# Optimization experiments

Hardware: AMD Instinct MI355X
Metric: run time of the kernel (lower is better)

Reference implementation:

```python
import jax, jax.numpy as jnp
import numpy as np

MOE_TOP_K = 2
MOE_GATE_NORM_STD = 1.0  # moe_gate_norm_std


def setup_inputs() -> dict:
    key = jax.random.key(0)
    k1, k2, k3, k4 = jax.random.split(key, 4)
    T, D, E = 16384, 2048, 8
    return {
        "x": jax.random.normal(k1, (T, D), dtype=jnp.float32),
        "wg_weight": jax.random.normal(k2, (E, D), dtype=jnp.float32) * 0.02,
        "gate_map_weight": jax.random.normal(k3, (E, E), dtype=jnp.float32) * 0.1,
        "gate_residual": jax.random.normal(k4, (T, E), dtype=jnp.float32),
    }


def reference(x, wg_weight, gate_map_weight, gate_residual):
    # Router GEMM in fp32 (module force-casts wg and input to float32)
    logits = jnp.einsum("td,ed->te", x.astype(jnp.float32), wg_weight)  # [T, E]
    # gate_residual path: gate_map Linear(E, E, bias=False)
    logits = logits + jnp.einsum("te,fe->tf", gate_residual, gate_map_weight)

    num_experts = wg_weight.shape[0]
    # gating(): moe_use_mixtral_gating=False, moe_use_logits_norm=True
    # torch.std is unbiased (ddof=1)
    logits_std = jnp.std(logits, axis=1, keepdims=True, ddof=1)
    probs = jax.nn.softmax(logits / (logits_std / MOE_GATE_NORM_STD), axis=1)
    gates, indices = jax.lax.top_k(probs, MOE_TOP_K)  # [T, K]
    # zero out routing to the last expert, then renormalize
    gates = jnp.where(indices == num_experts - 1, jnp.zeros_like(gates), gates)
    gates = gates / jnp.sum(gates, axis=1, keepdims=True)
    # Dense equivalent of the per-expert nonzero-gather dict: (indices, gates)
    # fully determines expert_info[e] = (tokens where indices==e, matching gates).
    return gates, indices, logits
```

## Files before the change

kernel.cpp:

```cpp
#include <hip/hip_runtime.h>
#include <hip/hip_bf16.h>
#include <stdint.h>


#define DCONST 2048
#define TOK_PER_BATCH 8
#define BATCHES 4

typedef float f32x4 __attribute__((ext_vector_type(4)));

__device__ __forceinline__ unsigned long long shfl_xor_u64(unsigned long long v, int m) {
    int lo = __shfl_xor((int)(uint32_t)v, m, 64);
    int hi = __shfl_xor((int)(uint32_t)(v >> 32), m, 64);
    return ((unsigned long long)(uint32_t)hi << 32) | (unsigned long long)(uint32_t)lo;
}

__global__ __launch_bounds__(256, 2)
void router_gemm(const float* __restrict__ x,
                 const float* __restrict__ wg,
                 float* __restrict__ ws,
                 int T)
{
    const int wave  = threadIdx.x >> 6;
    const int lane  = threadIdx.x & 63;
    const int W     = blockIdx.x * 4 + wave;
    const int g     = W & 7;
    const int tbase = (W >> 3) * 32;

    const float* wgp = wg + g * 256 + (lane << 2);
    f32x4 w8[8];
    #pragma unroll
    for (int e = 0; e < 8; ++e)
        w8[e] = *(const f32x4*)(wgp + (size_t)e * DCONST);

    const float* xp = x + (size_t)tbase * DCONST + g * 256 + (lane << 2);

    f32x4 xa[4], xb[4];

    #define LOADH(buf, trow)                                                  \
        { _Pragma("unroll")                                                   \
          for (int i = 0; i < 4; ++i)                                         \
              buf[i] = __builtin_nontemporal_load(                            \
                  (const f32x4*)(xp + (size_t)((trow) + i) * DCONST)); }

    #define FMAH(buf, tloc0)                                                  \
        { _Pragma("unroll")                                                   \
          for (int i = 0; i < 4; ++i) {                                       \
              _Pragma("unroll")                                               \
              for (int e = 0; e < 8; ++e) {                                   \
                  float a = acc[((tloc0) + i) * 8 + e];                       \
                  a += buf[i].x * w8[e].x;                                    \
                  a += buf[i].y * w8[e].y;                                    \
                  a += buf[i].z * w8[e].z;                                    \
                  a += buf[i].w * w8[e].w;                                    \
                  acc[((tloc0) + i) * 8 + e] = a;                             \
              }                                                               \
          } }

    LOADH(xa, 0);
    LOADH(xb, 4);

    #pragma unroll 1
    for (int b = 0; b < BATCHES; ++b) {
        float acc[64];
        #pragma unroll
        for (int v = 0; v < 64; ++v) acc[v] = 0.f;

        FMAH(xa, 0);
        if (b < BATCHES - 1) LOADH(xa, (b + 1) * 8);
        FMAH(xb, 4);
        if (b < BATCHES - 1) LOADH(xb, (b + 1) * 8 + 4);

        #pragma unroll
        for (int m = 1; m < 64; m <<= 1) {
            const bool up = (lane & m) != 0;
            #pragma unroll
            for (int v = 0; v < 64; v += 2 * m) {
                const float keep = up ? acc[v + m] : acc[v];
                const float send = up ? acc[v] : acc[v + m];
                const float got  = __shfl_xor(send, m, 64);
                acc[v] = keep + got;
            }
        }

        const int tb = (tbase + b * TOK_PER_BATCH) >> 3;
        ws[(size_t)tb * 512 + g * 64 + lane] = acc[0];
    }
}

__global__ __launch_bounds__(256)
void router_epilogue(const float* __restrict__ ws,
                     const float* __restrict__ gm,
                     const float* __restrict__ gr,
                     float* __restrict__ out,
                     int T)
{
    const int wave = threadIdx.x >> 6;
    const int lane = threadIdx.x & 63;
    const int tb   = blockIdx.x * 4 + wave;
    const int t0   = tb * 8;

    float logit = 0.f;
    #pragma unroll
    for (int g = 0; g < 8; ++g)
        logit += ws[(size_t)tb * 512 + g * 64 + lane];

    const int tt = lane >> 3;
    const int f  = lane & 7;
    const int t  = t0 + tt;

    const float4 ga = *(const float4*)(gr + (size_t)t * 8);
    const float4 gb = *(const float4*)(gr + (size_t)t * 8 + 4);
    const float4 ma = *(const float4*)(gm + f * 8);
    const float4 mb = *(const float4*)(gm + f * 8 + 4);
    logit += ga.x * ma.x + ga.y * ma.y + ga.z * ma.z + ga.w * ma.w
           + gb.x * mb.x + gb.y * mb.y + gb.z * mb.z + gb.w * mb.w;

    out[(size_t)4 * T + (size_t)t0 * 8 + lane] = logit;

    float s = logit;
    s += __shfl_xor(s, 1, 64);
    s += __shfl_xor(s, 2, 64);
    s += __shfl_xor(s, 4, 64);
    const float mean = s * 0.125f;
    float d2 = (logit - mean) * (logit - mean);
    d2 += __shfl_xor(d2, 1, 64);
    d2 += __shfl_xor(d2, 2, 64);
    d2 += __shfl_xor(d2, 4, 64);
    const float stdv = sqrtf(d2 / 7.0f);

    uint32_t ob = __float_as_uint(logit);
    ob = (ob & 0x80000000u) ? ~ob : (ob | 0x80000000u);
    unsigned long long k1 = ((unsigned long long)ob << 8) | (unsigned long long)(7 - f);
    unsigned long long k2 = 0ull;
    #pragma unroll
    for (int m = 1; m <= 4; m <<= 1) {
        const unsigned long long o1 = shfl_xor_u64(k1, m);
        const unsigned long long o2 = shfl_xor_u64(k2, m);
        const unsigned long long hi = k1 > o1 ? k1 : o1;
        const unsigned long long lo = k1 > o1 ? o1 : k1;
        const unsigned long long so = k2 > o2 ? k2 : o2;
        k1 = hi;
        k2 = lo > so ? lo : so;
    }
    const int i1 = 7 - (int)(k1 & 0xFFull);
    const int i2 = 7 - (int)(k2 & 0xFFull);
    uint32_t b1 = (uint32_t)(k1 >> 8), b2 = (uint32_t)(k2 >> 8);
    b1 = (b1 & 0x80000000u) ? (b1 ^ 0x80000000u) : ~b1;
    b2 = (b2 & 0x80000000u) ? (b2 ^ 0x80000000u) : ~b2;
    const float l1 = __uint_as_float(b1);
    const float l2 = __uint_as_float(b2);

    float g0, g1;
    if (i1 == 7)      { g0 = 0.f; g1 = 1.f; }
    else if (i2 == 7) { g0 = 1.f; g1 = 0.f; }
    else {
        const float p = 1.0f / (1.0f + __expf(-(l1 - l2) / stdv));
        g0 = p; g1 = 1.0f - p;
    }

    if (f == 0) out[(size_t)2 * t]             = g0;
    if (f == 1) out[(size_t)2 * t + 1]         = g1;
    if (f == 2) out[(size_t)2 * T + 2 * t]     = (float)i1;
    if (f == 3) out[(size_t)2 * T + 2 * t + 1] = (float)i2;
}

extern "C" void kernel_launch(void* const* d_in, const int* in_sizes, int n_in,
                              void* d_out, int out_size, void* d_ws, size_t ws_size,
                              hipStream_t stream) {
    const float* x  = (const float*)d_in[0];
    const float* wg = (const float*)d_in[1];
    const float* gm = (const float*)d_in[2];
    const float* gr = (const float*)d_in[3];
    float* ws = (float*)d_ws;
    const int T = in_sizes[0] / DCONST;

    const int gemm_blocks = (8 * (T / 32)) / 4;
    router_gemm<<<gemm_blocks, 256, 0, stream>>>(x, wg, ws, T);

    const int epi_blocks = T / 32;
    router_epilogue<<<epi_blocks, 256, 0, stream>>>(ws, gm, gr, (float*)d_out, T);
}
```

Baseline: 189.9 us.

## Make router GEMM persistent with two work items per wave and double-buffered 8-row loads

The router GEMM grid is cut to a fixed 512 blocks, and each wave loops over two work items spaced 2048 waves apart. Within a work item, loads are now double-buffered across two 8-row buffers, so the next batch's loads are issued before the current batch's FMAs and shuffle reduction. The aim is more memory requests in flight per wave and less launch/tail overhead. In exchange it uses more registers (16 f32x4 buffers plus 64 accumulators), which may lower occupancy, and the hardcoded grid and stride assume T=16384.

```diff
diff --git a/kernel.cpp b/kernel.cpp
--- a/kernel.cpp
+++ b/kernel.cpp
@@ -4,8 +4,6 @@
 
 
 #define DCONST 2048
-#define TOK_PER_BATCH 8
-#define BATCHES 4
 
 typedef float f32x4 __attribute__((ext_vector_type(4)));
 
@@ -21,70 +19,70 @@
                  float* __restrict__ ws,
                  int T)
 {
-    const int wave  = threadIdx.x >> 6;
-    const int lane  = threadIdx.x & 63;
-    const int W     = blockIdx.x * 4 + wave;
-    const int g     = W & 7;
-    const int tbase = (W >> 3) * 32;
-
-    const float* wgp = wg + g * 256 + (lane << 2);
-    f32x4 w8[8];
-    #pragma unroll
-    for (int e = 0; e < 8; ++e)
-        w8[e] = *(const f32x4*)(wgp + (size_t)e * DCONST);
-
-    const float* xp = x + (size_t)tbase * DCONST + g * 256 + (lane << 2);
-
-    f32x4 xa[4], xb[4];
-
-    #define LOADH(buf, trow)                                                  \
-        { _Pragma("unroll")                                                   \
-          for (int i = 0; i < 4; ++i)                                         \
-              buf[i] = __builtin_nontemporal_load(                            \
-                  (const f32x4*)(xp + (size_t)((trow) + i) * DCONST)); }
-
-    #define FMAH(buf, tloc0)                                                  \
-        { _Pragma("unroll")                                                   \
-          for (int i = 0; i < 4; ++i) {                                       \
-              _Pragma("unroll")                                               \
-              for (int e = 0; e < 8; ++e) {                                   \
-                  float a = acc[((tloc0) + i) * 8 + e];                       \
-                  a += buf[i].x * w8[e].x;                                    \
-                  a += buf[i].y * w8[e].y;                                    \
-                  a += buf[i].z * w8[e].z;                                    \
-                  a += buf[i].w * w8[e].w;                                    \
-                  acc[((tloc0) + i) * 8 + e] = a;                             \
-              }                                                               \
-          } }
-
-    LOADH(xa, 0);
-    LOADH(xb, 4);
+    const int wave = threadIdx.x >> 6;
+    const int lane = threadIdx.x & 63;
+    const int W    = blockIdx.x * 4 + wave;
 
     #pragma unroll 1
-    for (int b = 0; b < BATCHES; ++b) {
-        float acc[64];
+    for (int s = 0; s < 2; ++s) {
+        const int id    = W + s * 2048;
+        const int g     = id & 7;
+        const int trow  = (id >> 3) * 32;
+        const int tb0   = trow >> 3;
+
+        const float* wgp = wg + g * 256 + (lane << 2);
+        f32x4 w8[8];
         #pragma unroll
-        for (int v = 0; v < 64; ++v) acc[v] = 0.f;
+        for (int e = 0; e < 8; ++e)
+            w8[e] = *(const f32x4*)(wgp + (size_t)e * DCONST);
 
-        FMAH(xa, 0);
-        if (b < BATCHES - 1) LOADH(xa, (b + 1) * 8);
-        FMAH(xb, 4);
-        if (b < BATCHES - 1) LOADH(xb, (b + 1) * 8 + 4);
+        const float* xp = x + (size_t)trow * DCONST + g * 256 + (lane << 2);
 
-        #pragma unroll
-        for (int m = 1; m < 64; m <<= 1) {
-            const bool up = (lane & m) != 0;
-            #pragma unroll
-            for (int v = 0; v < 64; v += 2 * m) {
-                const float keep = up ? acc[v + m] : acc[v];
-                const float send = up ? acc[v] : acc[v + m];
-                const float got  = __shfl_xor(send, m, 64);
-                acc[v] = keep + got;
-            }
+        f32x4 A[8], B[8];
+
+        #define LOADB(buf, b)                                                 \
+            { _Pragma("unroll")                                               \
+              for (int i = 0; i < 8; ++i)                                     \
+                  buf[i] = __builtin_nontemporal_load(                        \
+                      (const f32x4*)(xp + (size_t)((b) * 8 + i) * DCONST)); }
+
+        #define DOBATCH(buf, b)                                               \
+            { float acc[64];                                                  \
+              _Pragma("unroll")                                               \
+              for (int v = 0; v < 64; ++v) acc[v] = 0.f;                      \
+              _Pragma("unroll")                                               \
+              for (int i = 0; i < 8; ++i) {                                   \
+                  _Pragma("unroll")                                           \
+                  for (int e = 0; e < 8; ++e) {                               \
+                      float a = acc[i * 8 + e];                               \
+                      a += buf[i].x * w8[e].x;                                \
+                      a += buf[i].y * w8[e].y;                                \
+                      a += buf[i].z * w8[e].z;                                \
+                      a += buf[i].w * w8[e].w;                                \
+                      acc[i * 8 + e] = a;                                     \
+                  }                                                           \
+              }                                                               \
+              _Pragma("unroll")                                               \
+              for (int m = 1; m < 64; m <<= 1) {                              \
+                  const bool up = (lane & m) != 0;                            \
+                  _Pragma("unroll")                                           \
+                  for (int v = 0; v < 64; v += 2 * m) {                       \
+                      const float keep = up ? acc[v + m] : acc[v];            \
+                      const float send = up ? acc[v] : acc[v + m];            \
+                      const float got  = __shfl_xor(send, m, 64);             \
+                      acc[v] = keep + got;                                    \
+                  }                                                           \
+              }                                                               \
+              ws[(size_t)(tb0 + (b)) * 512 + g * 64 + lane] = acc[0]; }
+
+        LOADB(A, 0);
+        #pragma unroll 1
+        for (int b = 0; b < 4; b += 2) {
+            LOADB(B, b + 1);
+            DOBATCH(A, b);
+            if (b + 2 < 4) LOADB(A, b + 2);
+            DOBATCH(B, b + 1);
         }
-
-        const int tb = (tbase + b * TOK_PER_BATCH) >> 3;
-        ws[(size_t)tb * 512 + g * 64 + lane] = acc[0];
     }
 }
 
@@ -175,8 +173,7 @@
     float* ws = (float*)d_ws;
     const int T = in_sizes[0] / DCONST;
 
-    const int gemm_blocks = (8 * (T / 32)) / 4;
-    router_gemm<<<gemm_blocks, 256, 0, stream>>>(x, wg, ws, T);
+    router_gemm<<<512, 256, 0, stream>>>(x, wg, ws, T);
 
     const int epi_blocks = T / 32;
     router_epilogue<<<epi_blocks, 256, 0, stream>>>(ws, gm, gr, (float*)d_out, T);
```

New measurement: 190.0 us. Within noise of the previous version (+0.0%).
